# Performance work log

Measured on AMD Instinct MI355X. Metric: run time of the kernel, lower is better.

Reference implementation:

```python
import jax, jax.numpy as jnp
import numpy as np

EMBED_DIM = 1024
NUM_HEADS = 16
HEAD_DIM = EMBED_DIM // NUM_HEADS


def setup_inputs() -> dict:
    key = jax.random.key(0)
    ks = jax.random.split(key, 9)
    B, S, E = 2, 2048, EMBED_DIM
    scale = 1.0 / np.sqrt(E)
    inp = {
        "x": jax.random.normal(ks[0], (B, S, E), dtype=jnp.float32),
        "Wq": jax.random.normal(ks[1], (E, E), dtype=jnp.float32) * scale,
        "bq": jnp.zeros((E,), dtype=jnp.float32),
        "Wk": jax.random.normal(ks[2], (E, E), dtype=jnp.float32) * scale,
        "bk": jnp.zeros((E,), dtype=jnp.float32),
        "Wv": jax.random.normal(ks[3], (E, E), dtype=jnp.float32) * scale,
        "bv": jnp.zeros((E,), dtype=jnp.float32),
        "Wo": jax.random.normal(ks[4], (E, E), dtype=jnp.float32) * scale,
        "bo": jnp.zeros((E,), dtype=jnp.float32),
    }
    return inp


def reference(x, Wq, bq, Wk, bk, Wv, bv, Wo, bo):
    B, S, E = x.shape
    H, D = NUM_HEADS, HEAD_DIM
    sm_scale = D ** (-0.5)

    def proj(W, b):
        # torch Linear: x @ W.T + b ; reshape to [B, H, S, D]
        y = jnp.einsum("bse,fe->bsf", x, W) + b
        return y.reshape(B, S, H, D).transpose(0, 2, 1, 3)

    q = proj(Wq, bq)  # [B, H, S, D]
    k = proj(Wk, bk)
    v = proj(Wv, bv)

    scores = jnp.einsum("bhqd,bhkd->bhqk", q, k) * sm_scale  # [B, H, S, S]
    attn = jax.nn.softmax(scores, axis=-1)
    o = jnp.einsum("bhqk,bhkd->bhqd", attn, v)  # [B, H, S, D]
    o = o.transpose(0, 2, 1, 3).reshape(B, S, E)
    return jnp.einsum("bse,fe->bsf", o, Wo) + bo
```

## Files before the change

### kernel.cpp

```cpp
#include <hip/hip_runtime.h>
#include <hip/hip_fp16.h>
#include <stdint.h>


typedef _Float16 f16;
typedef _Float16 f16x8 __attribute__((ext_vector_type(8)));
typedef _Float16 f16x4v __attribute__((ext_vector_type(4)));
typedef float f32x4 __attribute__((ext_vector_type(4)));
typedef int i32x4 __attribute__((ext_vector_type(4)));

#define BQ  2
#define SEQ 2048
#define EMB 1024
#define NH  16
#define HD  64
#define MM  (BQ * SEQ)

__device__ __forceinline__ void gld_lds16(const void* g, void* l) {
  __builtin_amdgcn_global_load_lds(
      (const __attribute__((address_space(1))) void*)g,
      (__attribute__((address_space(3))) void*)l, 16, 0, 0);
}

__device__ __forceinline__ void stage128x64(const f16* __restrict__ src,
                                            int ld, f16* lds, int tid) {
#pragma unroll
  for (int it = 0; it < 4; ++it) {
    int idx = it * 256 + tid;
    int r = idx >> 3, c = idx & 7;
    int sc = c ^ (r & 7);
    gld_lds16(src + (size_t)r * ld + sc * 8, lds + idx * 8);
  }
}

__device__ __forceinline__ f16x8 pack8(float a0, float a1, float a2, float a3,
                                       float b0, float b1, float b2, float b3) {
  i32x4 w;
  w.x = __builtin_bit_cast(int, __builtin_amdgcn_cvt_pkrtz(a0, a1));
  w.y = __builtin_bit_cast(int, __builtin_amdgcn_cvt_pkrtz(a2, a3));
  w.z = __builtin_bit_cast(int, __builtin_amdgcn_cvt_pkrtz(b0, b1));
  w.w = __builtin_bit_cast(int, __builtin_amdgcn_cvt_pkrtz(b2, b3));
  return __builtin_bit_cast(f16x8, w);
}

__global__ void cvt4(const float* __restrict__ src, f16* __restrict__ dst,
                     int n4) {
  int i = blockIdx.x * blockDim.x + threadIdx.x;
  if (i < n4) {
    float4 v = ((const float4*)src)[i];
    f16x4v o;
    o[0] = (f16)v.x; o[1] = (f16)v.y; o[2] = (f16)v.z; o[3] = (f16)v.w;
    ((f16x4v*)dst)[i] = o;
  }
}

__global__ void cvtW4(const float* __restrict__ s0, const float* __restrict__ s1,
                      const float* __restrict__ s2, const float* __restrict__ s3,
                      f16* __restrict__ d0, f16* __restrict__ d1,
                      f16* __restrict__ d2, f16* __restrict__ d3, int n4) {
  int i = blockIdx.x * blockDim.x + threadIdx.x;
  if (i >= n4) return;
  const float* s = (blockIdx.y == 0) ? s0 : (blockIdx.y == 1) ? s1
                   : (blockIdx.y == 2) ? s2 : s3;
  f16* d = (blockIdx.y == 0) ? d0 : (blockIdx.y == 1) ? d1
           : (blockIdx.y == 2) ? d2 : d3;
  float4 v = ((const float4*)s)[i];
  f16x4v o;
  o[0] = (f16)v.x; o[1] = (f16)v.y; o[2] = (f16)v.z; o[3] = (f16)v.w;
  ((f16x4v*)d)[i] = o;
}

template <int MODE>
__global__ __launch_bounds__(256, 2) void gemm_bt(
    const f16* __restrict__ A, const f16* __restrict__ W0,
    const f16* __restrict__ W1, const f16* __restrict__ W2,
    const float* __restrict__ b0, const float* __restrict__ b1,
    const float* __restrict__ b2, f16* __restrict__ o0, f16* __restrict__ o1,
    f16* __restrict__ o2, float* __restrict__ fo) {
  __shared__ __align__(16) f16 As[128 * 64];
  __shared__ __align__(16) f16 Bs[128 * 64];

  const int tid = threadIdx.x, lane = tid & 63, wid = tid >> 6;
  const int o = blockIdx.x;
  const int cx = o & 7, j = o >> 3;
  const int bx = 4 * cx + (j & 3);
  int by, z;
  if (MODE == 0) { int yz = j >> 2; by = yz & 7; z = yz >> 3; }
  else           { by = j >> 2; z = 0; }
  const f16* W = (z == 0) ? W0 : (z == 1 ? W1 : W2);
  const float* bia = (z == 0) ? b0 : (z == 1 ? b1 : b2);
  f16* outp = (z == 0) ? o0 : (z == 1 ? o1 : o2);
  const int row0 = bx * 128, col0 = by * 128;
  const int wr = (wid >> 1) * 64, wc = (wid & 1) * 64;
  const int rb = lane & 15, gq = lane >> 4, sw = lane & 7;

  f32x4 acc[4][4] = {};

  for (int kt = 0; kt < EMB / 64; ++kt) {
    __syncthreads();
    stage128x64(A + (size_t)row0 * EMB + kt * 64, EMB, As, tid);
    stage128x64(W + (size_t)col0 * EMB + kt * 64, EMB, Bs, tid);
    asm volatile("s_waitcnt vmcnt(0)" ::: "memory");
    __syncthreads();
#pragma unroll
    for (int kk = 0; kk < 2; ++kk) {
      f16x8 av[4], bv[4];
#pragma unroll
      for (int f = 0; f < 4; ++f) {
        av[f] = *(const f16x8*)(As + (wr + f * 16 + rb) * 64 +
                                (((kk * 4 + gq) ^ sw) << 3));
        bv[f] = *(const f16x8*)(Bs + (wc + f * 16 + rb) * 64 +
                                (((kk * 4 + gq) ^ sw) << 3));
      }
#pragma unroll
      for (int fi = 0; fi < 4; ++fi)
#pragma unroll
        for (int fj = 0; fj < 4; ++fj)
          acc[fi][fj] = __builtin_amdgcn_mfma_f32_16x16x32_f16(
              av[fi], bv[fj], acc[fi][fj], 0, 0, 0);
    }
  }

  float bias[4];
#pragma unroll
  for (int fj = 0; fj < 4; ++fj) bias[fj] = bia[col0 + wc + fj * 16 + rb];
  const float scale = (MODE == 0 && z == 0) ? 0.18033688011112042f : 1.0f;
#pragma unroll
  for (int fi = 0; fi < 4; ++fi) {
#pragma unroll
    for (int i = 0; i < 4; ++i) {
      int row = row0 + wr + fi * 16 + gq * 4 + i;
#pragma unroll
      for (int fj = 0; fj < 4; ++fj) {
        int col = col0 + wc + fj * 16 + rb;
        float v = (acc[fi][fj][i] + bias[fj]) * scale;
        if (MODE == 0) {
          int bb = row >> 11, s = row & (SEQ - 1);
          int h = col >> 6, d = col & 63;
          outp[(((size_t)(bb * NH + h)) * SEQ + s) * HD + d] = (f16)v;
        } else {
          fo[(size_t)row * EMB + col] = v;
        }
      }
    }
  }
}

__global__ __launch_bounds__(256) void vtrans(const f16* __restrict__ V,
                                              f16* __restrict__ Vt) {
  __shared__ f16 T[64][72];
  const int tid = threadIdx.x;
  const int s0 = blockIdx.x * 64, bh = blockIdx.y;
  const f16* Vh = V + (size_t)bh * SEQ * HD;
  f16* Vth = Vt + (size_t)bh * HD * SEQ;
#pragma unroll
  for (int it = 0; it < 2; ++it) {
    int idx = it * 256 + tid;
    int r = idx >> 3, c0 = (idx & 7) * 8;
    *(f16x8*)&T[r][c0] = *(const f16x8*)(Vh + (size_t)(s0 + r) * HD + c0);
  }
  __syncthreads();
#pragma unroll
  for (int it = 0; it < 2; ++it) {
    int idx = it * 256 + tid;
    int d = idx >> 3, a = idx & 7;
    f16x8 v;
#pragma unroll
    for (int j = 0; j < 8; ++j) v[j] = T[a * 8 + j][d];
    const int base = ((a >> 2) << 5) + ((a & 1) << 4) + (((a >> 1) & 1) << 2);
    f16* dst = Vth + (size_t)d * SEQ + s0 + base;
    f16x4v w0, w1;
#pragma unroll
    for (int j = 0; j < 4; ++j) { w0[j] = v[j]; w1[j] = v[4 + j]; }
    *(f16x4v*)dst = w0;
    *(f16x4v*)(dst + 8) = w1;
  }
}

__global__ __launch_bounds__(256, 2) void attn_fwd(const f16* __restrict__ Q,
                                                   const f16* __restrict__ K,
                                                   const f16* __restrict__ Vt,
                                                   f16* __restrict__ O) {
  __shared__ __align__(16) f16 Ks[2][2][64 * 64];
  __shared__ __align__(16) f16 Vs[2][2][64 * 64];

  const int tid = threadIdx.x, lane = tid & 63;
  const int wid = tid >> 6;
  const int orig = blockIdx.x;
  const int swz = ((orig & 7) << 6) + (orig >> 3);
  const int qt = swz & 15, bh = swz >> 4;
  const f16* Qh = Q + (size_t)bh * SEQ * HD;
  const f16* Kh = K + (size_t)bh * SEQ * HD;
  const f16* Vth = Vt + (size_t)bh * HD * SEQ;
  const int q0 = qt * 128 + wid * 32;
  const int rb = lane & 15, gq = lane >> 4, sw = lane & 7;

  f16x8 aq[2][2];
#pragma unroll
  for (int qf = 0; qf < 2; ++qf)
#pragma unroll
    for (int kk = 0; kk < 2; ++kk)
      aq[qf][kk] = *(const f16x8*)(Qh + (size_t)(q0 + qf * 16 + rb) * HD +
                                   kk * 32 + gq * 8);
  asm volatile("s_waitcnt vmcnt(0)" ::: "memory");

  const int srow = tid >> 3, scol = (tid & 7) ^ (srow & 7);
  const f16* Kg0 = Kh + (size_t)srow * HD + scol * 8;
  const f16* Vg0 = Vth + (size_t)srow * SEQ + scol * 8;

  const int NT2 = SEQ / 128;
#pragma unroll
  for (int sub = 0; sub < 2; ++sub) {
    const f16* kg = Kg0 + (size_t)sub * 64 * HD;
    const f16* vg = Vg0 + sub * 64;
    gld_lds16(kg,            &Ks[0][sub][tid * 8]);
    gld_lds16(kg + 32 * HD,  &Ks[0][sub][(tid + 256) * 8]);
    gld_lds16(vg,            &Vs[0][sub][tid * 8]);
    gld_lds16(vg + 32 * SEQ, &Vs[0][sub][(tid + 256) * 8]);
  }

  f32x4 oaccA[2][4] = {};
  f32x4 oaccB[2][4] = {};
  float lsum[2] = {0.f, 0.f};

  for (int t = 0; t < NT2; ++t) {
    __builtin_amdgcn_s_barrier();
    __builtin_amdgcn_sched_barrier(0);
    {
      const int tp = (t + 1 < NT2) ? t + 1 : NT2 - 1;
      const int ns = (t + 1) & 1;
#pragma unroll
      for (int sub = 0; sub < 2; ++sub) {
        const f16* kg = Kg0 + (size_t)(2 * tp + sub) * 64 * HD;
        const f16* vg = Vg0 + (2 * tp + sub) * 64;
        gld_lds16(kg,            &Ks[ns][sub][tid * 8]);
        gld_lds16(kg + 32 * HD,  &Ks[ns][sub][(tid + 256) * 8]);
        gld_lds16(vg,            &Vs[ns][sub][tid * 8]);
        gld_lds16(vg + 32 * SEQ, &Vs[ns][sub][(tid + 256) * 8]);
      }
      asm volatile("s_waitcnt vmcnt(8)" ::: "memory");
    }
    __builtin_amdgcn_s_barrier();
    __builtin_amdgcn_sched_barrier(0);

    const int cs = t & 1;
    const f16* Kb0 = &Ks[cs][0][0];
    const f16* Kb1 = &Ks[cs][1][0];
    const f16* Vb0 = &Vs[cs][0][0];
    const f16* Vb1 = &Vs[cs][1][0];

    __builtin_amdgcn_s_setprio(1);

    f32x4 s0_[2][4] = {};
#pragma unroll
    for (int kk = 0; kk < 2; ++kk) {
      f16x8 bk[4];
#pragma unroll
      for (int cf = 0; cf < 4; ++cf)
        bk[cf] = *(const f16x8*)(Kb0 + (cf * 16 + rb) * 64 +
                                 (((kk * 4 + gq) ^ sw) << 3));
#pragma unroll
      for (int qf = 0; qf < 2; ++qf)
#pragma unroll
        for (int cf = 0; cf < 4; ++cf)
          s0_[qf][cf] = __builtin_amdgcn_mfma_f32_16x16x32_f16(
              bk[cf], aq[qf][kk], s0_[qf][cf], 0, 0, 0);
    }

    f16x8 bp0[2][2];
#pragma unroll
    for (int qf = 0; qf < 2; ++qf)
#pragma unroll
      for (int g = 0; g < 2; ++g) {
        float e0 = __builtin_amdgcn_exp2f(s0_[qf][2 * g][0]);
        float e1 = __builtin_amdgcn_exp2f(s0_[qf][2 * g][1]);
        float e2 = __builtin_amdgcn_exp2f(s0_[qf][2 * g][2]);
        float e3 = __builtin_amdgcn_exp2f(s0_[qf][2 * g][3]);
        float f0 = __builtin_amdgcn_exp2f(s0_[qf][2 * g + 1][0]);
        float f1 = __builtin_amdgcn_exp2f(s0_[qf][2 * g + 1][1]);
        float f2 = __builtin_amdgcn_exp2f(s0_[qf][2 * g + 1][2]);
        float f3 = __builtin_amdgcn_exp2f(s0_[qf][2 * g + 1][3]);
        lsum[qf] += ((e0 + e1) + (e2 + e3)) + ((f0 + f1) + (f2 + f3));
        bp0[qf][g] = pack8(e0, e1, e2, e3, f0, f1, f2, f3);
      }

    f32x4 s1_[2][4] = {};
#pragma unroll
    for (int kk = 0; kk < 2; ++kk) {
      f16x8 bk[4];
#pragma unroll
      for (int cf = 0; cf < 4; ++cf)
        bk[cf] = *(const f16x8*)(Kb1 + (cf * 16 + rb) * 64 +
                                 (((kk * 4 + gq) ^ sw) << 3));
#pragma unroll
      for (int qf = 0; qf < 2; ++qf)
#pragma unroll
        for (int cf = 0; cf < 4; ++cf)
          s1_[qf][cf] = __builtin_amdgcn_mfma_f32_16x16x32_f16(
              bk[cf], aq[qf][kk], s1_[qf][cf], 0, 0, 0);
    }

#pragma unroll
    for (int g = 0; g < 2; ++g)
#pragma unroll
      for (int df = 0; df < 4; ++df) {
        f16x8 vb = *(const f16x8*)(Vb0 + (df * 16 + rb) * 64 +
                                   (((g * 4 + gq) ^ sw) << 3));
        oaccA[0][df] = __builtin_amdgcn_mfma_f32_16x16x32_f16(
            bp0[0][g], vb, oaccA[0][df], 0, 0, 0);
        oaccA[1][df] = __builtin_amdgcn_mfma_f32_16x16x32_f16(
            bp0[1][g], vb, oaccA[1][df], 0, 0, 0);
      }

    f16x8 bp1[2][2];
#pragma unroll
    for (int qf = 0; qf < 2; ++qf)
#pragma unroll
      for (int g = 0; g < 2; ++g) {
        float e0 = __builtin_amdgcn_exp2f(s1_[qf][2 * g][0]);
        float e1 = __builtin_amdgcn_exp2f(s1_[qf][2 * g][1]);
        float e2 = __builtin_amdgcn_exp2f(s1_[qf][2 * g][2]);
        float e3 = __builtin_amdgcn_exp2f(s1_[qf][2 * g][3]);
        float f0 = __builtin_amdgcn_exp2f(s1_[qf][2 * g + 1][0]);
        float f1 = __builtin_amdgcn_exp2f(s1_[qf][2 * g + 1][1]);
        float f2 = __builtin_amdgcn_exp2f(s1_[qf][2 * g + 1][2]);
        float f3 = __builtin_amdgcn_exp2f(s1_[qf][2 * g + 1][3]);
        lsum[qf] += ((e0 + e1) + (e2 + e3)) + ((f0 + f1) + (f2 + f3));
        bp1[qf][g] = pack8(e0, e1, e2, e3, f0, f1, f2, f3);
      }

#pragma unroll
    for (int g = 0; g < 2; ++g)
#pragma unroll
      for (int df = 0; df < 4; ++df) {
        f16x8 vb = *(const f16x8*)(Vb1 + (df * 16 + rb) * 64 +
                                   (((g * 4 + gq) ^ sw) << 3));
        oaccB[0][df] = __builtin_amdgcn_mfma_f32_16x16x32_f16(
            bp1[0][g], vb, oaccB[0][df], 0, 0, 0);
        oaccB[1][df] = __builtin_amdgcn_mfma_f32_16x16x32_f16(
            bp1[1][g], vb, oaccB[1][df], 0, 0, 0);
      }

    __builtin_amdgcn_s_setprio(0);
  }
  asm volatile("s_waitcnt vmcnt(0)" ::: "memory");

  float lv[2];
#pragma unroll
  for (int qf = 0; qf < 2; ++qf) {
    float l = lsum[qf];
    l += __shfl_xor(l, 16, 64);
    l += __shfl_xor(l, 32, 64);
    lv[qf] = l;
  }

  const int b = bh >> 4, h = bh & 15;
#pragma unroll
  for (int qf = 0; qf < 2; ++qf)
#pragma unroll
    for (int i = 0; i < 4; ++i) {
      const int rsel = (gq * 4 + i) & 15;
      const float l = __shfl(lv[qf], (lane & 48) + rsel, 64);
      const float inv = 1.0f / l;
      const int s = q0 + qf * 16 + gq * 4 + i;
      f16* orow = O + ((size_t)(b * SEQ + s)) * EMB + h * 64 + rb;
#pragma unroll
      for (int df = 0; df < 4; ++df)
        orow[df * 16] =
            (f16)((oaccA[qf][df][i] + oaccB[qf][df][i]) * inv);
    }
}

extern "C" void kernel_launch(void* const* d_in, const int* in_sizes, int n_in,
                              void* d_out, int out_size, void* d_ws,
                              size_t ws_size, hipStream_t stream) {
  const float* x = (const float*)d_in[0];
  const float* Wq = (const float*)d_in[1];
  const float* bq = (const float*)d_in[2];
  const float* Wk = (const float*)d_in[3];
  const float* bk = (const float*)d_in[4];
  const float* Wv = (const float*)d_in[5];
  const float* bv = (const float*)d_in[6];
  const float* Wo = (const float*)d_in[7];
  const float* bo = (const float*)d_in[8];
  float* out = (float*)d_out;

  const size_t NX = (size_t)MM * EMB;
  const size_t NW = (size_t)EMB * EMB;

  f16* xh  = (f16*)d_ws;
  f16* wqh = xh + NX;
  f16* wkh = wqh + NW;
  f16* wvh = wkh + NW;
  f16* woh = wvh + NW;
  f16* Qw  = woh + NW;
  f16* Kw  = Qw + NX;
  f16* Vw  = Kw + NX;
  f16* Vtw = Vw + NX;
  f16* Ow  = Vtw + NX;

  cvt4<<<(int)(NX / 4 / 256), 256, 0, stream>>>(x, xh, (int)(NX / 4));
  cvtW4<<<dim3((int)(NW / 4 / 256), 4), 256, 0, stream>>>(
      Wq, Wk, Wv, Wo, wqh, wkh, wvh, woh, (int)(NW / 4));

  gemm_bt<0><<<dim3(768), 256, 0, stream>>>(
      xh, wqh, wkh, wvh, bq, bk, bv, Qw, Kw, Vw, nullptr);

  vtrans<<<dim3(SEQ / 64, BQ * NH), 256, 0, stream>>>(Vw, Vtw);

  attn_fwd<<<dim3(512), 256, 0, stream>>>(Qw, Kw, Vtw, Ow);

  gemm_bt<1><<<dim3(256), 256, 0, stream>>>(
      Ow, woh, woh, woh, bo, bo, bo, nullptr, nullptr, nullptr, out);
}
```

Before: 106.7 us.

## Merge conversion kernels, double-buffer GEMM staging, fuse V transpose into projection

The two fp32-to-fp16 conversion kernels become one launch over a contiguous destination. The QKV and output GEMMs double-buffer their LDS tiles so the next k-tile's global loads overlap the current MFMA work, at the cost of twice the LDS per block. The V projection now writes its output directly in the transposed, permuted layout the attention kernel expects, which removes the separate vtrans kernel and its extra pass over V. Those scattered stores are strided across the sequence dimension and may coalesce poorly.

```diff
diff --git a/kernel.cpp b/kernel.cpp
--- a/kernel.cpp
+++ b/kernel.cpp
@@ -43,31 +43,24 @@
   return __builtin_bit_cast(f16x8, w);
 }
 
-__global__ void cvt4(const float* __restrict__ src, f16* __restrict__ dst,
-                     int n4) {
+__global__ void cvtAll(const float* __restrict__ x, const float* __restrict__ w0,
+                       const float* __restrict__ w1, const float* __restrict__ w2,
+                       const float* __restrict__ w3, f16* __restrict__ dst) {
   int i = blockIdx.x * blockDim.x + threadIdx.x;
-  if (i < n4) {
-    float4 v = ((const float4*)src)[i];
-    f16x4v o;
-    o[0] = (f16)v.x; o[1] = (f16)v.y; o[2] = (f16)v.z; o[3] = (f16)v.w;
-    ((f16x4v*)dst)[i] = o;
-  }
-}
-
-__global__ void cvtW4(const float* __restrict__ s0, const float* __restrict__ s1,
-                      const float* __restrict__ s2, const float* __restrict__ s3,
-                      f16* __restrict__ d0, f16* __restrict__ d1,
-                      f16* __restrict__ d2, f16* __restrict__ d3, int n4) {
-  int i = blockIdx.x * blockDim.x + threadIdx.x;
-  if (i >= n4) return;
-  const float* s = (blockIdx.y == 0) ? s0 : (blockIdx.y == 1) ? s1
-                   : (blockIdx.y == 2) ? s2 : s3;
-  f16* d = (blockIdx.y == 0) ? d0 : (blockIdx.y == 1) ? d1
-           : (blockIdx.y == 2) ? d2 : d3;
-  float4 v = ((const float4*)s)[i];
-  f16x4v o;
-  o[0] = (f16)v.x; o[1] = (f16)v.y; o[2] = (f16)v.z; o[3] = (f16)v.w;
-  ((f16x4v*)d)[i] = o;
+  const float* s;
+  int off;
+  if (i < (1 << 20)) {
+    s = x; off = i;
+  } else {
+    int j = i - (1 << 20);
+    int w = j >> 18, o = j & ((1 << 18) - 1);
+    s = (w == 0) ? w0 : (w == 1) ? w1 : (w == 2) ? w2 : w3;
+    off = o;
+  }
+  float4 v = ((const float4*)s)[off];
+  f16x4v out;
+  out[0] = (f16)v.x; out[1] = (f16)v.y; out[2] = (f16)v.z; out[3] = (f16)v.w;
+  ((f16x4v*)dst)[i] = out;
 }
 
 template <int MODE>
@@ -77,8 +70,8 @@
     const float* __restrict__ b0, const float* __restrict__ b1,
     const float* __restrict__ b2, f16* __restrict__ o0, f16* __restrict__ o1,
     f16* __restrict__ o2, float* __restrict__ fo) {
-  __shared__ __align__(16) f16 As[128 * 64];
-  __shared__ __align__(16) f16 Bs[128 * 64];
+  __shared__ __align__(16) f16 As[2][128 * 64];
+  __shared__ __align__(16) f16 Bs[2][128 * 64];
 
   const int tid = threadIdx.x, lane = tid & 63, wid = tid >> 6;
   const int o = blockIdx.x;
@@ -96,20 +89,33 @@
 
   f32x4 acc[4][4] = {};
 
-  for (int kt = 0; kt < EMB / 64; ++kt) {
-    __syncthreads();
-    stage128x64(A + (size_t)row0 * EMB + kt * 64, EMB, As, tid);
-    stage128x64(W + (size_t)col0 * EMB + kt * 64, EMB, Bs, tid);
-    asm volatile("s_waitcnt vmcnt(0)" ::: "memory");
-    __syncthreads();
+  const int NTK = EMB / 64;
+  stage128x64(A + (size_t)row0 * EMB, EMB, &As[0][0], tid);
+  stage128x64(W + (size_t)col0 * EMB, EMB, &Bs[0][0], tid);
+
+  for (int kt = 0; kt < NTK; ++kt) {
+    __builtin_amdgcn_s_barrier();
+    __builtin_amdgcn_sched_barrier(0);
+    {
+      const int tp = (kt + 1 < NTK) ? kt + 1 : NTK - 1;
+      const int ns = (kt + 1) & 1;
+      stage128x64(A + (size_t)row0 * EMB + tp * 64, EMB, &As[ns][0], tid);
+      stage128x64(W + (size_t)col0 * EMB + tp * 64, EMB, &Bs[ns][0], tid);
+      asm volatile("s_waitcnt vmcnt(8)" ::: "memory");
+    }
+    __builtin_amdgcn_s_barrier();
+    __builtin_amdgcn_sched_barrier(0);
+
+    const f16* Ab = &As[kt & 1][0];
+    const f16* Bb = &Bs[kt & 1][0];
 #pragma unroll
     for (int kk = 0; kk < 2; ++kk) {
       f16x8 av[4], bv[4];
 #pragma unroll
       for (int f = 0; f < 4; ++f) {
-        av[f] = *(const f16x8*)(As + (wr + f * 16 + rb) * 64 +
+        av[f] = *(const f16x8*)(Ab + (wr + f * 16 + rb) * 64 +
                                 (((kk * 4 + gq) ^ sw) << 3));
-        bv[f] = *(const f16x8*)(Bs + (wc + f * 16 + rb) * 64 +
+        bv[f] = *(const f16x8*)(Bb + (wc + f * 16 + rb) * 64 +
                                 (((kk * 4 + gq) ^ sw) << 3));
       }
 #pragma unroll
@@ -120,6 +126,7 @@
               av[fi], bv[fj], acc[fi][fj], 0, 0, 0);
     }
   }
+  asm volatile("s_waitcnt vmcnt(0)" ::: "memory");
 
   float bias[4];
 #pragma unroll
@@ -137,43 +144,20 @@
         if (MODE == 0) {
           int bb = row >> 11, s = row & (SEQ - 1);
           int h = col >> 6, d = col & 63;
-          outp[(((size_t)(bb * NH + h)) * SEQ + s) * HD + d] = (f16)v;
+          if (z == 2) {
+            int kv = s & 63;
+            int p = ((kv >> 5) << 5) + (((kv >> 2) & 3) << 3) +
+                    (((kv >> 4) & 1) << 2) + (kv & 3);
+            int spos = (s & ~63) | p;
+            outp[((size_t)(bb * NH + h) * HD + d) * SEQ + spos] = (f16)v;
+          } else {
+            outp[(((size_t)(bb * NH + h)) * SEQ + s) * HD + d] = (f16)v;
+          }
         } else {
           fo[(size_t)row * EMB + col] = v;
         }
       }
     }
-  }
-}
-
-__global__ __launch_bounds__(256) void vtrans(const f16* __restrict__ V,
-                                              f16* __restrict__ Vt) {
-  __shared__ f16 T[64][72];
-  const int tid = threadIdx.x;
-  const int s0 = blockIdx.x * 64, bh = blockIdx.y;
-  const f16* Vh = V + (size_t)bh * SEQ * HD;
-  f16* Vth = Vt + (size_t)bh * HD * SEQ;
-#pragma unroll
-  for (int it = 0; it < 2; ++it) {
-    int idx = it * 256 + tid;
-    int r = idx >> 3, c0 = (idx & 7) * 8;
-    *(f16x8*)&T[r][c0] = *(const f16x8*)(Vh + (size_t)(s0 + r) * HD + c0);
-  }
-  __syncthreads();
-#pragma unroll
-  for (int it = 0; it < 2; ++it) {
-    int idx = it * 256 + tid;
-    int d = idx >> 3, a = idx & 7;
-    f16x8 v;
-#pragma unroll
-    for (int j = 0; j < 8; ++j) v[j] = T[a * 8 + j][d];
-    const int base = ((a >> 2) << 5) + ((a & 1) << 4) + (((a >> 1) & 1) << 2);
-    f16* dst = Vth + (size_t)d * SEQ + s0 + base;
-    f16x4v w0, w1;
-#pragma unroll
-    for (int j = 0; j < 4; ++j) { w0[j] = v[j]; w1[j] = v[4 + j]; }
-    *(f16x4v*)dst = w0;
-    *(f16x4v*)(dst + 8) = w1;
   }
 }
 
@@ -395,18 +379,13 @@
   f16* woh = wvh + NW;
   f16* Qw  = woh + NW;
   f16* Kw  = Qw + NX;
-  f16* Vw  = Kw + NX;
-  f16* Vtw = Vw + NX;
+  f16* Vtw = Kw + NX;
   f16* Ow  = Vtw + NX;
 
-  cvt4<<<(int)(NX / 4 / 256), 256, 0, stream>>>(x, xh, (int)(NX / 4));
-  cvtW4<<<dim3((int)(NW / 4 / 256), 4), 256, 0, stream>>>(
-      Wq, Wk, Wv, Wo, wqh, wkh, wvh, woh, (int)(NW / 4));
+  cvtAll<<<dim3(8192), 256, 0, stream>>>(x, Wq, Wk, Wv, Wo, xh);
 
   gemm_bt<0><<<dim3(768), 256, 0, stream>>>(
-      xh, wqh, wkh, wvh, bq, bk, bv, Qw, Kw, Vw, nullptr);
-
-  vtrans<<<dim3(SEQ / 64, BQ * NH), 256, 0, stream>>>(Vw, Vtw);
+      xh, wqh, wkh, wvh, bq, bk, bv, Qw, Kw, Vtw, nullptr);
 
   attn_fwd<<<dim3(512), 256, 0, stream>>>(Qw, Kw, Vtw, Ow);
 
```

After: 115.4 us. 8.1% more time.
